# Optimization experiments

Hardware: AMD Instinct MI355X
Metric: run time of the kernel (lower is better)

The kernel has to match this reference:

```python
import jax, jax.numpy as jnp
import numpy as np

EPS_NORM = 1e-12
EPS_ENT = 1e-12
TEMPERATURE = 0.5
CONTRAST_DENOM = 128.0 * 100.0


def _l2_normalize(x, axis=-1):
    n = jnp.linalg.norm(x, axis=axis, keepdims=True)
    return x / jnp.maximum(n, EPS_NORM)


def setup_inputs() -> dict:
    key0 = jax.random.key(0)
    k1, k2, k3, k4 = jax.random.split(key0, 4)
    B, L, C = 16, 2048, 512
    M = 512
    return {
        "key": jax.random.normal(k1, (B, L, C), dtype=jnp.float32),
        "query": jax.random.normal(k2, (B, L, C), dtype=jnp.float32),
        "keys": jax.random.uniform(k3, (M, C), dtype=jnp.float32),
        "values": jax.random.uniform(k4, (M, C), dtype=jnp.float32),
        "mode": 0,
    }


def reference(key, query, keys, values, mode):
    B, L, C = key.shape
    k = _l2_normalize(key.reshape(-1, C))    # [T, C]
    q = _l2_normalize(query.reshape(-1, C))  # [T, C]

    # --- gatheringLoss ---
    score = jnp.einsum('tc,mc->tm', k, keys)            # [T, M]
    # top-1 of softmax(score) == argmax(score) (softmax is monotone)
    idx = jnp.argmax(score, axis=1)                     # [T]
    nearest_values = values[idx]                        # [T, C]
    gathering_loss = jnp.mean((q - nearest_values) ** 2)

    logits = score / TEMPERATURE                        # [T, M]
    logp = jax.nn.log_softmax(logits, axis=-1)
    gathered = jnp.take_along_axis(logp, idx[:, None], axis=1)  # [T, 1]
    contrast_loss = jnp.sum(gathered) / (-CONTRAST_DENOM)

    # --- read ---
    weights = jax.nn.softmax(score, axis=-1)            # [T, M]
    # EntropyLoss: mean over rows of -sum(w * log(w + eps))
    entropy_loss = jnp.mean(-jnp.sum(weights * jnp.log(weights + EPS_ENT), axis=-1))
    read_query = weights @ values                       # [T, C]

    return (read_query.reshape(B, L, C), entropy_loss, gathering_loss,
            contrast_loss, keys, values)
```

## Files before the change

### kernel.cpp

```cpp
#include <hip/hip_runtime.h>

typedef short short8 __attribute__((ext_vector_type(8)));
typedef float floatx4 __attribute__((ext_vector_type(4)));

#define C_DIM 512
#define KQ_STRIDE 1040

__device__ __forceinline__ unsigned short f2bf(float f) {
    unsigned u = __builtin_bit_cast(unsigned, f);
    u = u + 0x7fffu + ((u >> 16) & 1u);
    return (unsigned short)(u >> 16);
}

__global__ __launch_bounds__(256) void pack_kernel(
    const float* __restrict__ keys, const float* __restrict__ values,
    unsigned short* __restrict__ keysFrag, unsigned short* __restrict__ valsFrag) {
    int tid = blockIdx.x * 256 + threadIdx.x;
    int e  = tid & 32767;
    int l  = e & 63;
    int NT = (e >> 6) & 31;
    int kt = e >> 11;
    int li = l & 15, q4 = l >> 4;
    unsigned short tmp[8];
    if (tid < 32768) {
        const float* s = keys + (size_t)(NT * 16 + li) * C_DIM + kt * 32 + q4 * 8;
#pragma unroll
        for (int j = 0; j < 8; j++) tmp[j] = f2bf(s[j]);
        unsigned short* d = keysFrag + ((size_t)(kt * 32 + NT) * 64 + l) * 8;
        *(ushort4*)d       = make_ushort4(tmp[0], tmp[1], tmp[2], tmp[3]);
        *(ushort4*)(d + 4) = make_ushort4(tmp[4], tmp[5], tmp[6], tmp[7]);
    } else {
#pragma unroll
        for (int j = 0; j < 8; j++)
            tmp[j] = f2bf(values[(size_t)(kt * 32 + q4 * 8 + j) * C_DIM + NT * 16 + li]);
        unsigned short* d = valsFrag + ((size_t)(kt * 32 + NT) * 64 + l) * 8;
        *(ushort4*)d       = make_ushort4(tmp[0], tmp[1], tmp[2], tmp[3]);
        *(ushort4*)(d + 4) = make_ushort4(tmp[4], tmp[5], tmp[6], tmp[7]);
    }
}

__global__ __launch_bounds__(512, 4) void fused_kernel(
    const float* __restrict__ key,
    const float* __restrict__ query,
    const unsigned short* __restrict__ keysFrag,
    const unsigned short* __restrict__ valsFrag,
    const float* __restrict__ values,
    float* __restrict__ outRQ,
    float* __restrict__ scal) {
    __shared__ char kq[64 * KQ_STRIDE];
    __shared__ float stats[8][64][6];
    __shared__ float finals[64][2];
    __shared__ int   idxsh[64];
    __shared__ float gpart[8];

    const int tid = threadIdx.x;
    const int w  = tid >> 6;
    const int l  = tid & 63;
    const int li = l & 15;
    const int q4 = l >> 4;
    const int row0 = blockIdx.x << 6;

#pragma unroll
    for (int it = 0; it < 2; it++) {
        int r = (w << 3) + (it << 2) + q4;
        const float4* src = (const float4*)(key + (size_t)(row0 + r) * C_DIM);
        float4 v[8];
        float ss = 0.f;
#pragma unroll
        for (int i = 0; i < 8; i++) {
            v[i] = src[i * 16 + li];
            ss += v[i].x * v[i].x + v[i].y * v[i].y + v[i].z * v[i].z + v[i].w * v[i].w;
        }
#pragma unroll
        for (int m = 1; m < 16; m <<= 1) ss += __shfl_xor(ss, m, 64);
        float inv = 1.0f / fmaxf(sqrtf(ss), 1e-12f);
        char* dstrow = kq + r * KQ_STRIDE;
#pragma unroll
        for (int i = 0; i < 8; i++) {
            ushort4 b = make_ushort4(f2bf(v[i].x * inv), f2bf(v[i].y * inv),
                                     f2bf(v[i].z * inv), f2bf(v[i].w * inv));
            *(ushort4*)(dstrow + i * 128 + li * 8) = b;
        }
    }
    __syncthreads();

    floatx4 acc1[16];
#pragma unroll
    for (int i = 0; i < 16; i++) acc1[i] = (floatx4){0.f, 0.f, 0.f, 0.f};
    {
        const short8* kf = (const short8*)keysFrag;
        short8 bcur[4], bnxt[4];
#pragma unroll
        for (int nt = 0; nt < 4; nt++) bcur[nt] = kf[(size_t)((w * 4 + nt) * 64 + l)];
        for (int kt = 0; kt < 16; kt++) {
            if (kt < 15) {
#pragma unroll
                for (int nt = 0; nt < 4; nt++)
                    bnxt[nt] = kf[(size_t)(((kt + 1) * 32 + w * 4 + nt) * 64 + l)];
            }
            short8 a[4];
#pragma unroll
            for (int rg = 0; rg < 4; rg++)
                a[rg] = *(const short8*)(kq + (rg * 16 + li) * KQ_STRIDE + kt * 64 + q4 * 16);
#pragma unroll
            for (int rg = 0; rg < 4; rg++)
#pragma unroll
                for (int nt = 0; nt < 4; nt++)
                    acc1[rg * 4 + nt] = __builtin_amdgcn_mfma_f32_16x16x32_bf16(
                        a[rg], bcur[nt], acc1[rg * 4 + nt], 0, 0, 0);
#pragma unroll
            for (int nt = 0; nt < 4; nt++) bcur[nt] = bnxt[nt];
        }
    }

#pragma unroll
    for (int rg = 0; rg < 4; rg++) {
#pragma unroll
        for (int reg = 0; reg < 4; reg++) {
            float m = acc1[rg * 4][reg];
            int bi = w * 64 + li;
#pragma unroll
            for (int nt = 1; nt < 4; nt++) {
                float s = acc1[rg * 4 + nt][reg];
                if (s > m) { m = s; bi = w * 64 + nt * 16 + li; }
            }
            float z1 = 0.f, e1 = 0.f, z2 = 0.f;
#pragma unroll
            for (int nt = 0; nt < 4; nt++) {
                float s = acc1[rg * 4 + nt][reg];
                float p = __expf(s - m);
                z1 += p; e1 += p * s; z2 += p * p;
            }
#pragma unroll
            for (int msk = 1; msk < 16; msk <<= 1) {
                float mo  = __shfl_xor(m,  msk, 64);
                float z1o = __shfl_xor(z1, msk, 64);
                float e1o = __shfl_xor(e1, msk, 64);
                float z2o = __shfl_xor(z2, msk, 64);
                int   bio = __shfl_xor(bi, msk, 64);
                if (mo > m) {
                    float sc = __expf(m - mo);
                    z1 = z1 * sc + z1o; e1 = e1 * sc + e1o; z2 = z2 * sc * sc + z2o;
                    m = mo; bi = bio;
                } else if (mo == m) {
                    z1 += z1o; e1 += e1o; z2 += z2o; bi = min(bi, bio);
                } else {
                    float sc = __expf(mo - m);
                    z1 += z1o * sc; e1 += e1o * sc; z2 += z2o * sc * sc;
                }
            }
            if (li == 0) {
                float* st = stats[w][rg * 16 + q4 * 4 + reg];
                st[0] = m; st[1] = z1; st[2] = e1; st[3] = z2;
                ((int*)st)[4] = bi;
            }
        }
    }
    __syncthreads();

    if (tid < 64) {
        int r = tid;
        const float* st0 = stats[0][r];
        float m = st0[0], z1 = st0[1], e1 = st0[2], z2 = st0[3];
        int bi = ((const int*)st0)[4];
#pragma unroll
        for (int p = 1; p < 8; p++) {
            const float* st = stats[p][r];
            float mo = st[0], z1o = st[1], e1o = st[2], z2o = st[3];
            int bio = ((const int*)st)[4];
            if (mo > m) {
                float sc = __expf(m - mo);
                z1 = z1 * sc + z1o; e1 = e1 * sc + e1o; z2 = z2 * sc * sc + z2o;
                m = mo; bi = bio;
            } else if (mo == m) {
                z1 += z1o; e1 += e1o; z2 += z2o; bi = min(bi, bio);
            } else {
                float sc = __expf(mo - m);
                z1 += z1o * sc; e1 += e1o * sc; z2 += z2o * sc * sc;
            }
        }
        finals[r][0] = m;
        finals[r][1] = 1.0f / z1;
        idxsh[r] = bi;
        float ent = m + __logf(z1) - e1 / z1;
        float con = __logf(z2);
#pragma unroll
        for (int msk = 1; msk < 64; msk <<= 1) {
            ent += __shfl_xor(ent, msk, 64);
            con += __shfl_xor(con, msk, 64);
        }
        if (tid == 0) {
            atomicAdd(&scal[0], ent * (1.0f / 32768.0f));
            atomicAdd(&scal[2], con * (1.0f / 12800.0f));
        }
    }
    __syncthreads();

#pragma unroll
    for (int rg = 0; rg < 4; rg++) {
#pragma unroll
        for (int reg = 0; reg < 4; reg++) {
            int r = rg * 16 + q4 * 4 + reg;
            float m1 = finals[r][0];
#pragma unroll
            for (int nt = 0; nt < 4; nt++) {
                float p = __expf(acc1[rg * 4 + nt][reg] - m1);
                int col = w * 64 + nt * 16 + li;
                *(unsigned short*)(kq + r * KQ_STRIDE + col * 2) = f2bf(p);
            }
        }
    }
    __syncthreads();

    floatx4 acc2[16];
#pragma unroll
    for (int i = 0; i < 16; i++) acc2[i] = (floatx4){0.f, 0.f, 0.f, 0.f};
    {
        const short8* vf = (const short8*)valsFrag;
        short8 bcur[4], bnxt[4];
#pragma unroll
        for (int nt = 0; nt < 4; nt++) bcur[nt] = vf[(size_t)((w * 4 + nt) * 64 + l)];
        for (int kt = 0; kt < 16; kt++) {
            if (kt < 15) {
#pragma unroll
                for (int nt = 0; nt < 4; nt++)
                    bnxt[nt] = vf[(size_t)(((kt + 1) * 32 + w * 4 + nt) * 64 + l)];
            }
            short8 a[4];
#pragma unroll
            for (int rg = 0; rg < 4; rg++)
                a[rg] = *(const short8*)(kq + (rg * 16 + li) * KQ_STRIDE + kt * 64 + q4 * 16);
#pragma unroll
            for (int rg = 0; rg < 4; rg++)
#pragma unroll
                for (int nt = 0; nt < 4; nt++)
                    acc2[rg * 4 + nt] = __builtin_amdgcn_mfma_f32_16x16x32_bf16(
                        a[rg], bcur[nt], acc2[rg * 4 + nt], 0, 0, 0);
#pragma unroll
            for (int nt = 0; nt < 4; nt++) bcur[nt] = bnxt[nt];
        }
    }

#pragma unroll
    for (int rg = 0; rg < 4; rg++) {
#pragma unroll
        for (int reg = 0; reg < 4; reg++) {
            int r = rg * 16 + q4 * 4 + reg;
            float iz = finals[r][1];
            float* orow = outRQ + (size_t)(row0 + r) * C_DIM + w * 64 + li;
#pragma unroll
            for (int nt = 0; nt < 4; nt++) orow[nt * 16] = acc2[rg * 4 + nt][reg] * iz;
        }
    }

    float gacc = 0.f;
#pragma unroll
    for (int rr = 0; rr < 8; rr++) {
        int r = (w << 3) + rr;
        const float4* qr = (const float4*)(query + (size_t)(row0 + r) * C_DIM);
        float4 a = qr[l * 2], b = qr[l * 2 + 1];
        float ss = a.x * a.x + a.y * a.y + a.z * a.z + a.w * a.w +
                   b.x * b.x + b.y * b.y + b.z * b.z + b.w * b.w;
#pragma unroll
        for (int m = 1; m < 64; m <<= 1) ss += __shfl_xor(ss, m, 64);
        float inv = 1.0f / fmaxf(sqrtf(ss), 1e-12f);
        const float4* vr = (const float4*)(values + (size_t)idxsh[r] * C_DIM);
        float4 va = vr[l * 2], vb = vr[l * 2 + 1];
        float d;
        d = a.x * inv - va.x; gacc += d * d;
        d = a.y * inv - va.y; gacc += d * d;
        d = a.z * inv - va.z; gacc += d * d;
        d = a.w * inv - va.w; gacc += d * d;
        d = b.x * inv - vb.x; gacc += d * d;
        d = b.y * inv - vb.y; gacc += d * d;
        d = b.z * inv - vb.z; gacc += d * d;
        d = b.w * inv - vb.w; gacc += d * d;
    }
#pragma unroll
    for (int m = 1; m < 64; m <<= 1) gacc += __shfl_xor(gacc, m, 64);
    if (l == 0) gpart[w] = gacc;
    __syncthreads();
    if (tid == 0) {
        float s = 0.f;
#pragma unroll
        for (int i = 0; i < 8; i++) s += gpart[i];
        atomicAdd(&scal[1], s * (1.0f / (32768.0f * 512.0f)));
    }
}

extern "C" void kernel_launch(void* const* d_in, const int* in_sizes, int n_in,
                              void* d_out, int out_size, void* d_ws, size_t ws_size,
                              hipStream_t stream) {
    (void)in_sizes; (void)n_in; (void)out_size; (void)ws_size;
    const float* key    = (const float*)d_in[0];
    const float* query  = (const float*)d_in[1];
    const float* keysIn = (const float*)d_in[2];
    const float* valsIn = (const float*)d_in[3];
    float* out = (float*)d_out;

    unsigned short* keysFrag = (unsigned short*)d_ws;
    unsigned short* valsFrag = keysFrag + 512 * 512;

    float* outRQ   = out;
    float* scal    = out + 16777216;
    float* keysOut = out + 16777219;
    float* valsOut = keysOut + 262144;

    hipMemsetAsync(scal, 0, 3 * sizeof(float), stream);
    hipMemcpyAsync(keysOut, keysIn, 262144 * sizeof(float), hipMemcpyDeviceToDevice, stream);
    hipMemcpyAsync(valsOut, valsIn, 262144 * sizeof(float), hipMemcpyDeviceToDevice, stream);

    pack_kernel<<<256, 256, 0, stream>>>(keysIn, valsIn, keysFrag, valsFrag);
    fused_kernel<<<512, 512, 0, stream>>>(key, query, keysFrag, valsFrag, valsIn, outRQ, scal);
}
```

Before: 245.2 us.

## Drop max-shift in softmax stats, pack argmax into sortable key, fold copies into pack kernel

Scores are dot products of unit vectors with keys bounded in [0,1]^512, so the softmax is now computed without subtracting the row max. The exponentials are reused directly for the P·V matmul. Argmax is packed with its column index into one order-preserving uint key, so the cross-wave merge becomes plain sums and a max, and the separate single-wave reduction stage with its extra barrier is gone. The memset and two device copies are folded into the pack kernel to cut launch overhead. The risk is that dropping the max-shift relies on scores staying small enough for exp not to overflow, and the packed key loses the low 9 mantissa bits of the max score.

```diff
diff --git a/kernel.cpp b/kernel.cpp
--- a/kernel.cpp
+++ b/kernel.cpp
@@ -12,30 +12,49 @@
     return (unsigned short)(u >> 16);
 }
 
+__device__ __forceinline__ unsigned skey(float s, int col) {
+    unsigned u = __builtin_bit_cast(unsigned, s);
+    u = ((int)u < 0) ? ~u : (u | 0x80000000u);
+    return (u & ~0x1FFu) | (unsigned)(511 - col);
+}
+
 __global__ __launch_bounds__(256) void pack_kernel(
     const float* __restrict__ keys, const float* __restrict__ values,
-    unsigned short* __restrict__ keysFrag, unsigned short* __restrict__ valsFrag) {
+    unsigned short* __restrict__ keysFrag, unsigned short* __restrict__ valsFrag,
+    float* __restrict__ keysOut, float* __restrict__ valsOut,
+    float* __restrict__ scal) {
     int tid = blockIdx.x * 256 + threadIdx.x;
-    int e  = tid & 32767;
-    int l  = e & 63;
-    int NT = (e >> 6) & 31;
-    int kt = e >> 11;
-    int li = l & 15, q4 = l >> 4;
-    unsigned short tmp[8];
-    if (tid < 32768) {
-        const float* s = keys + (size_t)(NT * 16 + li) * C_DIM + kt * 32 + q4 * 8;
-#pragma unroll
-        for (int j = 0; j < 8; j++) tmp[j] = f2bf(s[j]);
-        unsigned short* d = keysFrag + ((size_t)(kt * 32 + NT) * 64 + l) * 8;
-        *(ushort4*)d       = make_ushort4(tmp[0], tmp[1], tmp[2], tmp[3]);
-        *(ushort4*)(d + 4) = make_ushort4(tmp[4], tmp[5], tmp[6], tmp[7]);
+    if (tid < 65536) {
+        int e  = tid & 32767;
+        int l  = e & 63;
+        int NT = (e >> 6) & 31;
+        int kt = e >> 11;
+        int li = l & 15, q4 = l >> 4;
+        unsigned short tmp[8];
+        if (tid < 32768) {
+            const float* s = keys + (size_t)(NT * 16 + li) * C_DIM + kt * 32 + q4 * 8;
+#pragma unroll
+            for (int j = 0; j < 8; j++) tmp[j] = f2bf(s[j]);
+            unsigned short* d = keysFrag + ((size_t)(kt * 32 + NT) * 64 + l) * 8;
+            *(ushort4*)d       = make_ushort4(tmp[0], tmp[1], tmp[2], tmp[3]);
+            *(ushort4*)(d + 4) = make_ushort4(tmp[4], tmp[5], tmp[6], tmp[7]);
+        } else {
+#pragma unroll
+            for (int j = 0; j < 8; j++)
+                tmp[j] = f2bf(values[(size_t)(kt * 32 + q4 * 8 + j) * C_DIM + NT * 16 + li]);
+            unsigned short* d = valsFrag + ((size_t)(kt * 32 + NT) * 64 + l) * 8;
+            *(ushort4*)d       = make_ushort4(tmp[0], tmp[1], tmp[2], tmp[3]);
+            *(ushort4*)(d + 4) = make_ushort4(tmp[4], tmp[5], tmp[6], tmp[7]);
+        }
     } else {
-#pragma unroll
-        for (int j = 0; j < 8; j++)
-            tmp[j] = f2bf(values[(size_t)(kt * 32 + q4 * 8 + j) * C_DIM + NT * 16 + li]);
-        unsigned short* d = valsFrag + ((size_t)(kt * 32 + NT) * 64 + l) * 8;
-        *(ushort4*)d       = make_ushort4(tmp[0], tmp[1], tmp[2], tmp[3]);
-        *(ushort4*)(d + 4) = make_ushort4(tmp[4], tmp[5], tmp[6], tmp[7]);
+        int ct = tid - 65536;
+        if (ct == 0) { scal[0] = 0.f; scal[1] = 0.f; scal[2] = 0.f; }
+#pragma unroll
+        for (int i = 0; i < 4; i++) {
+            int idx = ct + i * 32768;
+            if (idx < 65536) ((float4*)keysOut)[idx] = ((const float4*)keys)[idx];
+            else             ((float4*)valsOut)[idx - 65536] = ((const float4*)values)[idx - 65536];
+        }
     }
 }
 
@@ -48,9 +67,7 @@
     float* __restrict__ outRQ,
     float* __restrict__ scal) {
     __shared__ char kq[64 * KQ_STRIDE];
-    __shared__ float stats[8][64][6];
-    __shared__ float finals[64][2];
-    __shared__ int   idxsh[64];
+    __shared__ __align__(16) float stats[8][64][4];
     __shared__ float gpart[8];
 
     const int tid = threadIdx.x;
@@ -117,81 +134,40 @@
     for (int rg = 0; rg < 4; rg++) {
 #pragma unroll
         for (int reg = 0; reg < 4; reg++) {
-            float m = acc1[rg * 4][reg];
-            int bi = w * 64 + li;
-#pragma unroll
-            for (int nt = 1; nt < 4; nt++) {
-                float s = acc1[rg * 4 + nt][reg];
-                if (s > m) { m = s; bi = w * 64 + nt * 16 + li; }
-            }
-            float z1 = 0.f, e1 = 0.f, z2 = 0.f;
-#pragma unroll
-            for (int nt = 0; nt < 4; nt++) {
-                float s = acc1[rg * 4 + nt][reg];
-                float p = __expf(s - m);
-                z1 += p; e1 += p * s; z2 += p * p;
-            }
+            const int colbase = (w << 6) + li;
+            float s0 = acc1[rg * 4 + 0][reg];
+            float s1 = acc1[rg * 4 + 1][reg];
+            float s2 = acc1[rg * 4 + 2][reg];
+            float s3 = acc1[rg * 4 + 3][reg];
+            unsigned K  = skey(s0, colbase);
+            unsigned K1 = skey(s1, colbase + 16);
+            unsigned K2 = skey(s2, colbase + 32);
+            unsigned K3 = skey(s3, colbase + 48);
+            K = K1 > K ? K1 : K;
+            K = K2 > K ? K2 : K;
+            K = K3 > K ? K3 : K;
+            float p0 = __expf(s0), p1 = __expf(s1), p2 = __expf(s2), p3 = __expf(s3);
+            float z1 = (p0 + p1) + (p2 + p3);
+            float e1 = p0 * s0 + p1 * s1 + p2 * s2 + p3 * s3;
+            float z2 = p0 * p0 + p1 * p1 + p2 * p2 + p3 * p3;
+            acc1[rg * 4 + 0][reg] = p0;
+            acc1[rg * 4 + 1][reg] = p1;
+            acc1[rg * 4 + 2][reg] = p2;
+            acc1[rg * 4 + 3][reg] = p3;
 #pragma unroll
             for (int msk = 1; msk < 16; msk <<= 1) {
-                float mo  = __shfl_xor(m,  msk, 64);
-                float z1o = __shfl_xor(z1, msk, 64);
-                float e1o = __shfl_xor(e1, msk, 64);
-                float z2o = __shfl_xor(z2, msk, 64);
-                int   bio = __shfl_xor(bi, msk, 64);
-                if (mo > m) {
-                    float sc = __expf(m - mo);
-                    z1 = z1 * sc + z1o; e1 = e1 * sc + e1o; z2 = z2 * sc * sc + z2o;
-                    m = mo; bi = bio;
-                } else if (mo == m) {
-                    z1 += z1o; e1 += e1o; z2 += z2o; bi = min(bi, bio);
-                } else {
-                    float sc = __expf(mo - m);
-                    z1 += z1o * sc; e1 += e1o * sc; z2 += z2o * sc * sc;
-                }
+                unsigned Ko = __shfl_xor(K, msk, 64);
+                z1 += __shfl_xor(z1, msk, 64);
+                e1 += __shfl_xor(e1, msk, 64);
+                z2 += __shfl_xor(z2, msk, 64);
+                K = Ko > K ? Ko : K;
             }
             if (li == 0) {
-                float* st = stats[w][rg * 16 + q4 * 4 + reg];
-                st[0] = m; st[1] = z1; st[2] = e1; st[3] = z2;
-                ((int*)st)[4] = bi;
-            }
-        }
-    }
-    __syncthreads();
-
-    if (tid < 64) {
-        int r = tid;
-        const float* st0 = stats[0][r];
-        float m = st0[0], z1 = st0[1], e1 = st0[2], z2 = st0[3];
-        int bi = ((const int*)st0)[4];
-#pragma unroll
-        for (int p = 1; p < 8; p++) {
-            const float* st = stats[p][r];
-            float mo = st[0], z1o = st[1], e1o = st[2], z2o = st[3];
-            int bio = ((const int*)st)[4];
-            if (mo > m) {
-                float sc = __expf(m - mo);
-                z1 = z1 * sc + z1o; e1 = e1 * sc + e1o; z2 = z2 * sc * sc + z2o;
-                m = mo; bi = bio;
-            } else if (mo == m) {
-                z1 += z1o; e1 += e1o; z2 += z2o; bi = min(bi, bio);
-            } else {
-                float sc = __expf(mo - m);
-                z1 += z1o * sc; e1 += e1o * sc; z2 += z2o * sc * sc;
-            }
-        }
-        finals[r][0] = m;
-        finals[r][1] = 1.0f / z1;
-        idxsh[r] = bi;
-        float ent = m + __logf(z1) - e1 / z1;
-        float con = __logf(z2);
-#pragma unroll
-        for (int msk = 1; msk < 64; msk <<= 1) {
-            ent += __shfl_xor(ent, msk, 64);
-            con += __shfl_xor(con, msk, 64);
-        }
-        if (tid == 0) {
-            atomicAdd(&scal[0], ent * (1.0f / 32768.0f));
-            atomicAdd(&scal[2], con * (1.0f / 12800.0f));
+                floatx4 sv;
+                sv[0] = __builtin_bit_cast(float, K);
+                sv[1] = z1; sv[2] = e1; sv[3] = z2;
+                *(floatx4*)stats[w][rg * 16 + q4 * 4 + reg] = sv;
+            }
         }
     }
     __syncthreads();
@@ -201,12 +177,10 @@
 #pragma unroll
         for (int reg = 0; reg < 4; reg++) {
             int r = rg * 16 + q4 * 4 + reg;
-            float m1 = finals[r][0];
 #pragma unroll
             for (int nt = 0; nt < 4; nt++) {
-                float p = __expf(acc1[rg * 4 + nt][reg] - m1);
-                int col = w * 64 + nt * 16 + li;
-                *(unsigned short*)(kq + r * KQ_STRIDE + col * 2) = f2bf(p);
+                int col = (w << 6) + nt * 16 + li;
+                *(unsigned short*)(kq + r * KQ_STRIDE + col * 2) = f2bf(acc1[rg * 4 + nt][reg]);
             }
         }
     }
@@ -241,15 +215,30 @@
         }
     }
 
+    unsigned K; float z1, e1, z2;
+    {
+        floatx4 v = *(const floatx4*)stats[0][l];
+        K = __builtin_bit_cast(unsigned, v[0]); z1 = v[1]; e1 = v[2]; z2 = v[3];
+#pragma unroll
+        for (int p = 1; p < 8; p++) {
+            floatx4 u = *(const floatx4*)stats[p][l];
+            unsigned Ko = __builtin_bit_cast(unsigned, u[0]);
+            K = Ko > K ? Ko : K;
+            z1 += u[1]; e1 += u[2]; z2 += u[3];
+        }
+    }
+    const float iz = 1.0f / z1;
+    const int myidx = 511 - (int)(K & 0x1FFu);
+
 #pragma unroll
     for (int rg = 0; rg < 4; rg++) {
 #pragma unroll
         for (int reg = 0; reg < 4; reg++) {
             int r = rg * 16 + q4 * 4 + reg;
-            float iz = finals[r][1];
-            float* orow = outRQ + (size_t)(row0 + r) * C_DIM + w * 64 + li;
-#pragma unroll
-            for (int nt = 0; nt < 4; nt++) orow[nt * 16] = acc2[rg * 4 + nt][reg] * iz;
+            float izr = __shfl(iz, r, 64);
+            float* orow = outRQ + (size_t)(row0 + r) * C_DIM + (w << 6) + li;
+#pragma unroll
+            for (int nt = 0; nt < 4; nt++) orow[nt * 16] = acc2[rg * 4 + nt][reg] * izr;
         }
     }
 
@@ -257,6 +246,7 @@
 #pragma unroll
     for (int rr = 0; rr < 8; rr++) {
         int r = (w << 3) + rr;
+        int idxr = __shfl(myidx, r, 64);
         const float4* qr = (const float4*)(query + (size_t)(row0 + r) * C_DIM);
         float4 a = qr[l * 2], b = qr[l * 2 + 1];
         float ss = a.x * a.x + a.y * a.y + a.z * a.z + a.w * a.w +
@@ -264,7 +254,7 @@
 #pragma unroll
         for (int m = 1; m < 64; m <<= 1) ss += __shfl_xor(ss, m, 64);
         float inv = 1.0f / fmaxf(sqrtf(ss), 1e-12f);
-        const float4* vr = (const float4*)(values + (size_t)idxsh[r] * C_DIM);
+        const float4* vr = (const float4*)(values + (size_t)idxr * C_DIM);
         float4 va = vr[l * 2], vb = vr[l * 2 + 1];
         float d;
         d = a.x * inv - va.x; gacc += d * d;
@@ -279,6 +269,23 @@
 #pragma unroll
     for (int m = 1; m < 64; m <<= 1) gacc += __shfl_xor(gacc, m, 64);
     if (l == 0) gpart[w] = gacc;
+
+    if (w == 0) {
+        unsigned um = (K >> 31) ? (K & 0x7FFFFFFFu) : ~K;
+        um &= ~0x1FFu;
+        float m1 = __builtin_bit_cast(float, um);
+        float ent = __logf(z1) - e1 * iz;
+        float con = __logf(z2) - 2.0f * m1;
+#pragma unroll
+        for (int msk = 1; msk < 64; msk <<= 1) {
+            ent += __shfl_xor(ent, msk, 64);
+            con += __shfl_xor(con, msk, 64);
+        }
+        if (l == 0) {
+            atomicAdd(&scal[0], ent * (1.0f / 32768.0f));
+            atomicAdd(&scal[2], con * (1.0f / 12800.0f));
+        }
+    }
     __syncthreads();
     if (tid == 0) {
         float s = 0.f;
@@ -306,10 +313,7 @@
     float* keysOut = out + 16777219;
     float* valsOut = keysOut + 262144;
 
-    hipMemsetAsync(scal, 0, 3 * sizeof(float), stream);
-    hipMemcpyAsync(keysOut, keysIn, 262144 * sizeof(float), hipMemcpyDeviceToDevice, stream);
-    hipMemcpyAsync(valsOut, valsIn, 262144 * sizeof(float), hipMemcpyDeviceToDevice, stream);
-
-    pack_kernel<<<256, 256, 0, stream>>>(keysIn, valsIn, keysFrag, valsFrag);
+    pack_kernel<<<384, 256, 0, stream>>>(keysIn, valsIn, keysFrag, valsFrag,
+                                         keysOut, valsOut, scal);
     fused_kernel<<<512, 512, 0, stream>>>(key, query, keysFrag, valsFrag, valsIn, outRQ, scal);
 }
```

New measurement: 245.1 us. About the same (-0.1%).
